# Optimization experiments

Measured on AMD Instinct MI355X. Metric: run time of the kernel, lower is better.

Reference implementation:

```python
import jax, jax.numpy as jnp
import numpy as np
import math

NDIM = 16
SCALE = math.sqrt(1.0 / NDIM)


def setup_inputs() -> dict:
    key = jax.random.key(0)
    ks = jax.random.split(key, 7)
    L, Bsz, Dm = 4096, 4, 1024
    return {
        "x": jax.random.normal(ks[0], (L, Bsz, Dm), dtype=jnp.float32),
        "log_dt": jax.random.normal(ks[1], (Dm, 1), dtype=jnp.float32),
        "log_A_real": jax.random.normal(ks[2], (Dm, NDIM), dtype=jnp.float32),
        "A_imag": jax.random.normal(ks[3], (Dm, NDIM), dtype=jnp.float32),
        "B": jax.random.normal(ks[4], (Dm, NDIM, 2), dtype=jnp.float32),
        "C": jax.random.normal(ks[5], (Dm, NDIM, 2), dtype=jnp.float32),
        "D_param": jax.random.normal(ks[6], (Dm,), dtype=jnp.float32),
    }


def _compute_kernel(log_dt, log_A_real, A_imag, B, C, length):
    dt = jnp.exp(log_dt)                                  # (D,1)
    A = -jnp.exp(log_A_real) + 1j * A_imag                # (D,N) complex
    dtA = A * dt                                          # (D,N)
    Cc = (B[..., 0] + 1j * B[..., 1]) * (C[..., 0] + 1j * C[..., 1])  # (D,N)
    # bilinear discretization
    p = Cc * dt / (1.0 - dtA / 2)                         # (D,N)
    log_q = jnp.log((1.0 + dtA / 2) / (1.0 - dtA / 2))    # (D,N)
    # Vandermonde: (D,N,L) complex — the kernel-gen bottleneck
    vander = jnp.exp(jnp.arange(length)[None, None, :] * log_q[:, :, None])
    k = jnp.einsum('dnl,dn->dl', vander, p * SCALE).real  # (D,L)
    return k


def reference(x, log_dt, log_A_real, A_imag, B, C, D_param):
    seq_len, bsz, dim = x.shape
    residual = x * D_param                                # (L,B,D)
    xt = jnp.transpose(x, (1, 2, 0))                      # (B,D,L)
    k = _compute_kernel(log_dt, log_A_real, A_imag, B, C, seq_len)
    fft_len = 2 * seq_len
    k_f = jnp.fft.rfft(k.astype(jnp.float32), n=fft_len)  # (D, fft_len//2+1)
    x_f = jnp.fft.rfft(xt.astype(jnp.float32), n=fft_len)  # (B,D, fft_len//2+1)
    out = jnp.fft.irfft(x_f * k_f, n=fft_len)[..., :seq_len]  # (B,D,L)
    out = out.astype(x.dtype)
    return jax.nn.silu(jnp.transpose(out, (2, 0, 1)) + residual)
```

## Files before the change

kernel.cpp:

```cpp
#include <hip/hip_runtime.h>
#include <math.h>

#define L_SEQ  4096
#define BSZ    4
#define DM     1024
#define NS     16
#define NSH    8
#define NCHUNK 64
#define CHUNK  (L_SEQ / NCHUNK)
#define LOG2_CHUNK 6
#define SCALE  0.25f
#define LBD    (BSZ * DM)


__global__ void s4d_params(const float* __restrict__ log_dt,
                           const float* __restrict__ log_A_real,
                           const float* __restrict__ A_imag,
                           const float* __restrict__ Bp,
                           const float* __restrict__ Cp,
                           float2* __restrict__ qbuf,
                           float2* __restrict__ pbuf) {
    int t = blockIdx.x * blockDim.x + threadIdx.x;
    if (t >= NS * DM) return;
    int n = t >> 10, d = t & (DM - 1);
    int i = d * NS + n;
    float dt = expf(log_dt[d]);
    float Ar = -expf(log_A_real[i]);
    float Ai = A_imag[i];
    float ar = 0.5f * Ar * dt, ai = 0.5f * Ai * dt;
    float den_r = 1.0f - ar, den_i = -ai;
    float num_r = 1.0f + ar, num_i = ai;
    float inv = 1.0f / (den_r * den_r + den_i * den_i);
    float qr = (num_r * den_r + num_i * den_i) * inv;
    float qi = (num_i * den_r - num_r * den_i) * inv;
    float B0 = Bp[2 * i], B1 = Bp[2 * i + 1];
    float C0 = Cp[2 * i], C1 = Cp[2 * i + 1];
    float ccr = B0 * C0 - B1 * C1;
    float cci = B0 * C1 + B1 * C0;
    float s = dt * inv * SCALE;
    float pr = (ccr * den_r + cci * den_i) * s;
    float pi = (cci * den_r - ccr * den_i) * s;
    qbuf[t] = make_float2(qr, qi);
    pbuf[t] = make_float2(pr, pi);
}

__global__ __launch_bounds__(256, 4)
void s4d_pass1(const float* __restrict__ x,
               const float2* __restrict__ qbuf,
               float2* __restrict__ S) {
    int tid  = blockIdx.x * 256 + threadIdx.x;
    int lane = tid & 63;
    int dlo  = lane & 31;
    int half = lane >> 5;
    int u    = tid >> 6;
    int dhi  = u & 31;
    int bc   = u >> 5;
    int c    = bc & (NCHUNK - 1);
    int d    = dhi * 32 + dlo;
    int b    = bc >> LOG2_CHUNK;
    int nb   = half * NSH;

    float qr[NSH], qi[NSH], hr[NSH], hi[NSH];
#pragma unroll
    for (int j = 0; j < NSH; ++j) {
        float2 v = qbuf[(nb + j) * DM + d];
        qr[j] = v.x; qi[j] = v.y; hr[j] = 0.0f; hi[j] = 0.0f;
    }
    const float* xp = x + (size_t)(c * CHUNK) * LBD + b * DM + d;
#pragma unroll 4
    for (int l = 0; l < CHUNK; ++l) {
        float xv = xp[(size_t)l * LBD];
#pragma unroll
        for (int j = 0; j < NSH; ++j) {
            float nr = fmaf(qr[j], hr[j], fmaf(-qi[j], hi[j], xv));
            float ni = fmaf(qr[j], hi[j], qi[j] * hr[j]);
            hr[j] = nr; hi[j] = ni;
        }
    }
    float2* sp = S + ((size_t)bc * NS + nb) * DM + d;
#pragma unroll
    for (int j = 0; j < NSH; ++j) sp[(size_t)j * DM] = make_float2(hr[j], hi[j]);
}

__global__ __launch_bounds__(256)
void s4d_pass2(const float2* __restrict__ qbuf,
               float2* __restrict__ S) {
    int tid = blockIdx.x * 256 + threadIdx.x;
    int d = tid & (DM - 1);
    int n = (tid >> 10) & (NS - 1);
    int b = tid >> 14;
    float2 qv = qbuf[n * DM + d];
    float qr = qv.x, qi = qv.y;
#pragma unroll
    for (int i = 0; i < LOG2_CHUNK; ++i) {
        float nr = qr * qr - qi * qi;
        float ni = 2.0f * qr * qi;
        qr = nr; qi = ni;
    }
    size_t base = ((size_t)b * NCHUNK * NS + n) * DM + d;
    const size_t cs = (size_t)NS * DM;
    float hr = 0.0f, hi = 0.0f;
    float2 s0 = S[base + 0 * cs], s1 = S[base + 1 * cs],
           s2 = S[base + 2 * cs], s3 = S[base + 3 * cs],
           s4 = S[base + 4 * cs], s5 = S[base + 5 * cs],
           s6 = S[base + 6 * cs], s7 = S[base + 7 * cs];
#pragma unroll
    for (int c0 = 0; c0 < NCHUNK; c0 += 8) {
        float2 t0, t1, t2, t3, t4, t5, t6, t7;
        if (c0 + 8 < NCHUNK) {
            size_t nb2 = base + (size_t)(c0 + 8) * cs;
            t0 = S[nb2 + 0 * cs]; t1 = S[nb2 + 1 * cs];
            t2 = S[nb2 + 2 * cs]; t3 = S[nb2 + 3 * cs];
            t4 = S[nb2 + 4 * cs]; t5 = S[nb2 + 5 * cs];
            t6 = S[nb2 + 6 * cs]; t7 = S[nb2 + 7 * cs];
        }
#define STEP(J, SB)                                                      \
        {                                                                \
            S[base + (size_t)(c0 + J) * cs] = make_float2(hr, hi);       \
            float nr = fmaf(qr, hr, fmaf(-qi, hi, SB.x));                \
            float ni = fmaf(qr, hi, fmaf(qi, hr, SB.y));                 \
            hr = nr; hi = ni;                                            \
        }
        STEP(0, s0) STEP(1, s1) STEP(2, s2) STEP(3, s3)
        STEP(4, s4) STEP(5, s5) STEP(6, s6) STEP(7, s7)
#undef STEP
        if (c0 + 8 < NCHUNK) {
            s0 = t0; s1 = t1; s2 = t2; s3 = t3;
            s4 = t4; s5 = t5; s6 = t6; s7 = t7;
        }
    }
}

__global__ __launch_bounds__(256, 4)
void s4d_pass3(const float* __restrict__ x,
               const float* __restrict__ Dp,
               const float2* __restrict__ qbuf,
               const float2* __restrict__ pbuf,
               const float2* __restrict__ S,
               float* __restrict__ out) {
    int tid  = blockIdx.x * 256 + threadIdx.x;
    int lane = tid & 63;
    int dlo  = lane & 31;
    int half = lane >> 5;
    int u    = tid >> 6;
    int dhi  = u & 31;
    int bc   = u >> 5;
    int c    = bc & (NCHUNK - 1);
    int d    = dhi * 32 + dlo;
    int b    = bc >> LOG2_CHUNK;
    int nb   = half * NSH;

    float qr[NSH], qi[NSH], pr[NSH], pi[NSH], hr[NSH], hi[NSH];
#pragma unroll
    for (int j = 0; j < NSH; ++j) {
        float2 v = qbuf[(nb + j) * DM + d];
        float2 w = pbuf[(nb + j) * DM + d];
        qr[j] = v.x; qi[j] = v.y; pr[j] = w.x; pi[j] = w.y;
    }
    const float2* sp = S + ((size_t)bc * NS + nb) * DM + d;
#pragma unroll
    for (int j = 0; j < NSH; ++j) {
        float2 s = sp[(size_t)j * DM];
        hr[j] = s.x; hi[j] = s.y;
    }
    float dpar = Dp[d];
    const float* xp = x + (size_t)(c * CHUNK) * LBD + b * DM + d;
    float* op = out + (size_t)(c * CHUNK) * LBD + b * DM + d;
#pragma unroll 2
    for (int l = 0; l < CHUNK; ++l) {
        float xv = xp[(size_t)l * LBD];
        float acc = 0.0f;
#pragma unroll
        for (int j = 0; j < NSH; ++j) {
            float nr = fmaf(qr[j], hr[j], fmaf(-qi[j], hi[j], xv));
            float ni = fmaf(qr[j], hi[j], qi[j] * hr[j]);
            hr[j] = nr; hi[j] = ni;
            acc = fmaf(pr[j], nr, fmaf(-pi[j], ni, acc));
        }
        acc += __shfl_xor(acc, 32, 64);
        float z = fmaf(xv, dpar, acc);
        float sig = 1.0f / (1.0f + expf(-z));
        if (half == 0) op[(size_t)l * LBD] = z * sig;
    }
}

extern "C" void kernel_launch(void* const* d_in, const int* in_sizes, int n_in,
                              void* d_out, int out_size, void* d_ws, size_t ws_size,
                              hipStream_t stream) {
    const float* x          = (const float*)d_in[0];
    const float* log_dt     = (const float*)d_in[1];
    const float* log_A_real = (const float*)d_in[2];
    const float* A_imag     = (const float*)d_in[3];
    const float* Bp         = (const float*)d_in[4];
    const float* Cp         = (const float*)d_in[5];
    const float* Dp         = (const float*)d_in[6];
    float* out = (float*)d_out;

    float2* qbuf = (float2*)d_ws;
    float2* pbuf = qbuf + NS * DM;
    float2* S    = pbuf + NS * DM;

    hipLaunchKernelGGL(s4d_params, dim3((NS * DM) / 256), dim3(256), 0, stream,
                       log_dt, log_A_real, A_imag, Bp, Cp, qbuf, pbuf);
    hipLaunchKernelGGL(s4d_pass1, dim3((2 * BSZ * NCHUNK * DM) / 256), dim3(256), 0, stream,
                       x, qbuf, S);
    hipLaunchKernelGGL(s4d_pass2, dim3((BSZ * DM * NS) / 256), dim3(256), 0, stream,
                       qbuf, S);
    hipLaunchKernelGGL(s4d_pass3, dim3((2 * BSZ * NCHUNK * DM) / 256), dim3(256), 0, stream,
                       x, Dp, qbuf, pbuf, S, out);
}
```

Baseline: 219.5 us.

## Process all 16 states per thread in scan passes, batch x loads

Passes 1 and 3 now give each thread all 16 SSM states for one (b,chunk,d), instead of splitting the states across two half-wavefronts that were combined with a cross-lane shuffle. This halves the grid, removes the shuffle and the redundant x loads and sigmoid work in the idle half, and fully unrolls the chunk loop with 8 x values loaded at a time. Pass 3 also switches to the fast __expf. The cost is higher register pressure from 96 live floats in pass 3 and the dropped occupancy hint, which may lower occupancy and reduce latency hiding for the strided x loads.

```diff
diff --git a/kernel.cpp b/kernel.cpp
--- a/kernel.cpp
+++ b/kernel.cpp
@@ -5,7 +5,6 @@
 #define BSZ    4
 #define DM     1024
 #define NS     16
-#define NSH    8
 #define NCHUNK 64
 #define CHUNK  (L_SEQ / NCHUNK)
 #define LOG2_CHUNK 6
@@ -39,47 +38,47 @@
     float cci = B0 * C1 + B1 * C0;
     float s = dt * inv * SCALE;
     float pr = (ccr * den_r + cci * den_i) * s;
-    float pi = (cci * den_r - ccr * den_i) * s;
+    float pi = (cci * den_r - cci * 0.0f - ccr * den_i) * s;
+    pbuf[t] = make_float2(pr, pi);
     qbuf[t] = make_float2(qr, qi);
-    pbuf[t] = make_float2(pr, pi);
-}
-
-__global__ __launch_bounds__(256, 4)
+}
+
+__global__ __launch_bounds__(256)
 void s4d_pass1(const float* __restrict__ x,
                const float2* __restrict__ qbuf,
                float2* __restrict__ S) {
-    int tid  = blockIdx.x * 256 + threadIdx.x;
-    int lane = tid & 63;
-    int dlo  = lane & 31;
-    int half = lane >> 5;
-    int u    = tid >> 6;
-    int dhi  = u & 31;
-    int bc   = u >> 5;
-    int c    = bc & (NCHUNK - 1);
-    int d    = dhi * 32 + dlo;
-    int b    = bc >> LOG2_CHUNK;
-    int nb   = half * NSH;
-
-    float qr[NSH], qi[NSH], hr[NSH], hi[NSH];
-#pragma unroll
-    for (int j = 0; j < NSH; ++j) {
-        float2 v = qbuf[(nb + j) * DM + d];
-        qr[j] = v.x; qi[j] = v.y; hr[j] = 0.0f; hi[j] = 0.0f;
+    int tid = blockIdx.x * 256 + threadIdx.x;
+    int d  = tid & (DM - 1);
+    int bc = tid >> 10;
+    int c  = bc & (NCHUNK - 1);
+    int b  = bc >> LOG2_CHUNK;
+
+    float qr[NS], qi[NS], hr[NS], hi[NS];
+#pragma unroll
+    for (int n = 0; n < NS; ++n) {
+        float2 v = qbuf[n * DM + d];
+        qr[n] = v.x; qi[n] = v.y; hr[n] = 0.0f; hi[n] = 0.0f;
     }
     const float* xp = x + (size_t)(c * CHUNK) * LBD + b * DM + d;
-#pragma unroll 4
-    for (int l = 0; l < CHUNK; ++l) {
-        float xv = xp[(size_t)l * LBD];
-#pragma unroll
-        for (int j = 0; j < NSH; ++j) {
-            float nr = fmaf(qr[j], hr[j], fmaf(-qi[j], hi[j], xv));
-            float ni = fmaf(qr[j], hi[j], qi[j] * hr[j]);
-            hr[j] = nr; hi[j] = ni;
-        }
-    }
-    float2* sp = S + ((size_t)bc * NS + nb) * DM + d;
-#pragma unroll
-    for (int j = 0; j < NSH; ++j) sp[(size_t)j * DM] = make_float2(hr[j], hi[j]);
+#pragma unroll
+    for (int l0 = 0; l0 < CHUNK; l0 += 8) {
+        float xv[8];
+#pragma unroll
+        for (int j = 0; j < 8; ++j)
+            xv[j] = xp[(size_t)(l0 + j) * LBD];
+#pragma unroll
+        for (int j = 0; j < 8; ++j) {
+#pragma unroll
+            for (int n = 0; n < NS; ++n) {
+                float nr = fmaf(qr[n], hr[n], fmaf(-qi[n], hi[n], xv[j]));
+                float ni = fmaf(qr[n], hi[n], qi[n] * hr[n]);
+                hr[n] = nr; hi[n] = ni;
+            }
+        }
+    }
+    float2* sp = S + (size_t)bc * NS * DM + d;
+#pragma unroll
+    for (int n = 0; n < NS; ++n) sp[(size_t)n * DM] = make_float2(hr[n], hi[n]);
 }
 
 __global__ __launch_bounds__(256)
@@ -131,56 +130,55 @@
     }
 }
 
-__global__ __launch_bounds__(256, 4)
+__global__ __launch_bounds__(256)
 void s4d_pass3(const float* __restrict__ x,
                const float* __restrict__ Dp,
                const float2* __restrict__ qbuf,
                const float2* __restrict__ pbuf,
                const float2* __restrict__ S,
                float* __restrict__ out) {
-    int tid  = blockIdx.x * 256 + threadIdx.x;
-    int lane = tid & 63;
-    int dlo  = lane & 31;
-    int half = lane >> 5;
-    int u    = tid >> 6;
-    int dhi  = u & 31;
-    int bc   = u >> 5;
-    int c    = bc & (NCHUNK - 1);
-    int d    = dhi * 32 + dlo;
-    int b    = bc >> LOG2_CHUNK;
-    int nb   = half * NSH;
-
-    float qr[NSH], qi[NSH], pr[NSH], pi[NSH], hr[NSH], hi[NSH];
-#pragma unroll
-    for (int j = 0; j < NSH; ++j) {
-        float2 v = qbuf[(nb + j) * DM + d];
-        float2 w = pbuf[(nb + j) * DM + d];
-        qr[j] = v.x; qi[j] = v.y; pr[j] = w.x; pi[j] = w.y;
-    }
-    const float2* sp = S + ((size_t)bc * NS + nb) * DM + d;
-#pragma unroll
-    for (int j = 0; j < NSH; ++j) {
-        float2 s = sp[(size_t)j * DM];
-        hr[j] = s.x; hi[j] = s.y;
+    int tid = blockIdx.x * 256 + threadIdx.x;
+    int d  = tid & (DM - 1);
+    int bc = tid >> 10;
+    int c  = bc & (NCHUNK - 1);
+    int b  = bc >> LOG2_CHUNK;
+
+    float qr[NS], qi[NS], pr[NS], pi[NS], hr[NS], hi[NS];
+#pragma unroll
+    for (int n = 0; n < NS; ++n) {
+        float2 v = qbuf[n * DM + d];
+        float2 w = pbuf[n * DM + d];
+        qr[n] = v.x; qi[n] = v.y; pr[n] = w.x; pi[n] = w.y;
+    }
+    const float2* sp = S + (size_t)bc * NS * DM + d;
+#pragma unroll
+    for (int n = 0; n < NS; ++n) {
+        float2 s = sp[(size_t)n * DM];
+        hr[n] = s.x; hi[n] = s.y;
     }
     float dpar = Dp[d];
     const float* xp = x + (size_t)(c * CHUNK) * LBD + b * DM + d;
     float* op = out + (size_t)(c * CHUNK) * LBD + b * DM + d;
-#pragma unroll 2
-    for (int l = 0; l < CHUNK; ++l) {
-        float xv = xp[(size_t)l * LBD];
-        float acc = 0.0f;
-#pragma unroll
-        for (int j = 0; j < NSH; ++j) {
-            float nr = fmaf(qr[j], hr[j], fmaf(-qi[j], hi[j], xv));
-            float ni = fmaf(qr[j], hi[j], qi[j] * hr[j]);
-            hr[j] = nr; hi[j] = ni;
-            acc = fmaf(pr[j], nr, fmaf(-pi[j], ni, acc));
-        }
-        acc += __shfl_xor(acc, 32, 64);
-        float z = fmaf(xv, dpar, acc);
-        float sig = 1.0f / (1.0f + expf(-z));
-        if (half == 0) op[(size_t)l * LBD] = z * sig;
+#pragma unroll
+    for (int l0 = 0; l0 < CHUNK; l0 += 8) {
+        float xv[8];
+#pragma unroll
+        for (int j = 0; j < 8; ++j)
+            xv[j] = xp[(size_t)(l0 + j) * LBD];
+#pragma unroll
+        for (int j = 0; j < 8; ++j) {
+            float acc = 0.0f;
+#pragma unroll
+            for (int n = 0; n < NS; ++n) {
+                float nr = fmaf(qr[n], hr[n], fmaf(-qi[n], hi[n], xv[j]));
+                float ni = fmaf(qr[n], hi[n], qi[n] * hr[n]);
+                hr[n] = nr; hi[n] = ni;
+                acc = fmaf(pr[n], nr, fmaf(-pi[n], ni, acc));
+            }
+            float z = fmaf(xv[j], dpar, acc);
+            float sig = 1.0f / (1.0f + __expf(-z));
+            op[(size_t)(l0 + j) * LBD] = z * sig;
+        }
     }
 }
 
@@ -202,10 +200,10 @@
 
     hipLaunchKernelGGL(s4d_params, dim3((NS * DM) / 256), dim3(256), 0, stream,
                        log_dt, log_A_real, A_imag, Bp, Cp, qbuf, pbuf);
-    hipLaunchKernelGGL(s4d_pass1, dim3((2 * BSZ * NCHUNK * DM) / 256), dim3(256), 0, stream,
+    hipLaunchKernelGGL(s4d_pass1, dim3((BSZ * NCHUNK * DM) / 256), dim3(256), 0, stream,
                        x, qbuf, S);
     hipLaunchKernelGGL(s4d_pass2, dim3((BSZ * DM * NS) / 256), dim3(256), 0, stream,
                        qbuf, S);
-    hipLaunchKernelGGL(s4d_pass3, dim3((2 * BSZ * NCHUNK * DM) / 256), dim3(256), 0, stream,
+    hipLaunchKernelGGL(s4d_pass3, dim3((BSZ * NCHUNK * DM) / 256), dim3(256), 0, stream,
                        x, Dp, qbuf, pbuf, S, out);
 }
```

Result: slower. 247.7 us (+12.8%).
